# Kernel tuning notes

Hardware: AMD Instinct MI355X
Metric: run time of the kernel (lower is better)

Reference implementation:

```python
import jax, jax.numpy as jnp
import numpy as np

N_NODES = 50000
N_EDGES = 640000
D = 128
N_RELS = 16
N_NTYPES = 8


def setup_inputs() -> dict:
    key = jax.random.key(0)
    ks = jax.random.split(key, 9)
    return {
        "feats": jax.random.normal(ks[0], (N_NODES, D), dtype=jnp.float32),
        "W_edge": jax.random.normal(ks[1], (N_RELS, D, D), dtype=jnp.float32) / np.sqrt(D),
        "b_edge": jax.random.normal(ks[2], (N_RELS, D), dtype=jnp.float32) * 0.02,
        "W_node": jax.random.normal(ks[3], (N_NTYPES, D, D), dtype=jnp.float32) / np.sqrt(D),
        "b_node": jax.random.normal(ks[4], (N_NTYPES, D), dtype=jnp.float32) * 0.02,
        "src": jax.random.randint(ks[5], (N_EDGES,), 0, N_NODES, dtype=jnp.int32),
        "dst": jax.random.randint(ks[6], (N_EDGES,), 0, N_NODES, dtype=jnp.int32),
        "ntypes": jax.random.randint(ks[7], (N_NODES,), 0, N_NTYPES, dtype=jnp.int32),
        "etypes": jax.random.randint(ks[8], (N_EDGES,), 0, N_RELS, dtype=jnp.int32),
    }


def reference(feats, W_edge, b_edge, W_node, b_node, src, dst, ntypes, etypes):
    N, d = feats.shape
    T = W_edge.shape[0]
    # Per-relation linear applied to all nodes once: [T, N, out]; then gather per edge.
    hW = jnp.einsum('nd,tdf->tnf', feats, W_edge) + b_edge[:, None, :]
    msg = hW[etypes, src]  # [E, out]
    # Per-(dst-node, edge-type) in-degree counts (one_hot count normalization).
    seg = dst * T + etypes  # [E]
    counts = jax.ops.segment_sum(jnp.ones(msg.shape[0], dtype=msg.dtype), seg,
                                 num_segments=N * T)  # [N*T]
    msg = msg / counts[seg][:, None]
    # Scatter-sum messages into destination nodes (zero for isolated nodes).
    agg = jax.ops.segment_sum(msg, dst, num_segments=N)  # [N, out]
    # Type-conditional node transform + residual message + activation.
    hN = jnp.einsum('nd,tdf->tnf', feats, W_node) + b_node[:, None, :]  # [Tn, N, out]
    out = hN[ntypes, jnp.arange(N)] + agg
    return jax.nn.relu(out)
```

## Files before the change

kernel.cpp:

```cpp
#include <hip/hip_runtime.h>
#include <hip/hip_bf16.h>
#include <stdint.h>


#define D 128
#define TRELS 16
#define NTYPES 8

typedef __bf16 bf16x8 __attribute__((ext_vector_type(8)));
typedef float f32x4 __attribute__((ext_vector_type(4)));
typedef unsigned int u32x4 __attribute__((ext_vector_type(4)));

__device__ __forceinline__ unsigned short f2bf(float f) {
  union { float f; unsigned u; } v; v.f = f;
  unsigned u = v.u;
  return (unsigned short)((u + 0x7FFFu + ((u >> 16) & 1u)) >> 16);
}
__device__ __forceinline__ float bf2f(unsigned short h) {
  union { unsigned u; float f; } v; v.u = ((unsigned)h) << 16;
  return v.f;
}

__global__ void prep_k(const float* __restrict__ feats,
                       const float* __restrict__ We,
                       const float* __restrict__ Wn,
                       unsigned short* __restrict__ featsbf,
                       unsigned short* __restrict__ WeT,
                       unsigned short* __restrict__ WnT,
                       int nfeat) {
  int idx = blockIdx.x * 256 + threadIdx.x;
  if (idx < nfeat) { featsbf[idx] = f2bf(feats[idx]); return; }
  idx -= nfeat;
  if (idx < TRELS * D * D) {
    int t = idx >> 14, rem = idx & 16383;
    int n = rem >> 7, k = rem & 127;
    WeT[idx] = f2bf(We[t * 16384 + k * 128 + n]);
    return;
  }
  idx -= TRELS * D * D;
  if (idx < NTYPES * D * D) {
    int t = idx >> 14, rem = idx & 16383;
    int n = rem >> 7, k = rem & 127;
    WnT[idx] = f2bf(Wn[t * 16384 + k * 128 + n]);
  }
}

__global__ void hist_k(const int* __restrict__ src, const int* __restrict__ dst,
                       const int* __restrict__ etypes,
                       const int* __restrict__ ntypes, int E, int N,
                       int* __restrict__ cnt, int* __restrict__ nhist,
                       int* __restrict__ srcuse) {
  __shared__ int sh_n[NTYPES];
  int tid = threadIdx.x;
  if (tid < NTYPES) sh_n[tid] = 0;
  __syncthreads();
  int g = blockIdx.x * 256 + tid;
  if (g < E) {
    int et = etypes[g];
    atomicAdd(&cnt[dst[g] * TRELS + et], 1);
    atomicOr(&srcuse[src[g]], 1 << et);
  }
  if (g < N) atomicAdd(&sh_n[ntypes[g]], 1);
  __syncthreads();
  if (tid < NTYPES && sh_n[tid]) atomicAdd(&nhist[tid], sh_n[tid]);
}

__global__ void scan1_k(const int* __restrict__ cnt, int* __restrict__ doff,
                        int* __restrict__ bsum, int N) {
  __shared__ int sd[256];
  int b = blockIdx.x, tid = threadIdx.x;
  int base = b * 1024 + tid * 4;
  int v[4]; int tot = 0;
  for (int j = 0; j < 4; ++j) {
    int i = base + j;
    int dg = 0;
    if (i < N) {
      const int* row = cnt + i * TRELS;
#pragma unroll
      for (int et = 0; et < TRELS; ++et) dg += row[et];
    }
    v[j] = tot; tot += dg;
  }
  sd[tid] = tot;
  __syncthreads();
  for (int off = 1; off < 256; off <<= 1) {
    int t = (tid >= off) ? sd[tid - off] : 0;
    __syncthreads();
    sd[tid] += t;
    __syncthreads();
  }
  int excl = sd[tid] - tot;
  for (int j = 0; j < 4; ++j) {
    int i = base + j;
    if (i < N) doff[i] = excl + v[j];
  }
  if (tid == 255) bsum[b] = sd[255];
}

__global__ void scan2_k(int* __restrict__ misc, int* __restrict__ bsum, int nb) {
  if (threadIdx.x != 0) return;
  int run = 0;
  for (int b = 0; b < nb; ++b) { int t = bsum[b]; bsum[b] = run; run += t; }
  int* noff = misc; int* ntb = misc + 9; int* ncur = misc + 18; int* nhist = misc + 26;
  int s = 0, ts = 0;
  for (int t = 0; t < NTYPES; ++t) {
    noff[t] = s; ncur[t] = s; ntb[t] = ts;
    s += nhist[t]; ts += (nhist[t] + 127) >> 7;
  }
  noff[NTYPES] = s; ntb[NTYPES] = ts;
}

__global__ void scan3_k(int* __restrict__ doff, int* __restrict__ dcur,
                        const int* __restrict__ bsum, int N, int E) {
  int b = blockIdx.x, tid = threadIdx.x;
  int add = bsum[b];
  int base = b * 1024 + tid * 4;
  for (int j = 0; j < 4; ++j) {
    int i = base + j;
    if (i < N) { int o = doff[i] + add; doff[i] = o; dcur[i] = o; }
  }
  if (b == 0 && tid == 0) doff[N] = E;
}

__global__ void scatter_k(const int* __restrict__ src, const int* __restrict__ dst,
                          const int* __restrict__ etypes, const int* __restrict__ ntypes,
                          int E, int N, int* __restrict__ misc,
                          int* __restrict__ dcur,
                          int* __restrict__ edst, int* __restrict__ nsorted) {
  __shared__ int lc_n[NTYPES], lb_n[NTYPES];
  int tid = threadIdx.x;
  if (tid < NTYPES) lc_n[tid] = 0;
  __syncthreads();
  int g = blockIdx.x * 256 + tid;
  if (g < E) {
    int d = dst[g];
    int pos = atomicAdd(&dcur[d], 1);
    edst[pos] = src[g] * TRELS + etypes[g];
  }
  int tn = -1, idn = 0;
  if (g < N) { tn = ntypes[g]; idn = atomicAdd(&lc_n[tn], 1); }
  __syncthreads();
  if (tid < NTYPES && lc_n[tid]) lb_n[tid] = atomicAdd(&misc[18 + tid], lc_n[tid]);
  __syncthreads();
  if (g < N) nsorted[lb_n[tn] + idn] = g;
}

__global__ __launch_bounds__(256) void hw_gemm_k(
    const unsigned short* __restrict__ featsbf,
    const unsigned short* __restrict__ WeT,
    const int* __restrict__ srcuse,
    unsigned short* __restrict__ hW, int N, int mtiles) {
  __shared__ unsigned char Asm[128 * 264];
  __shared__ unsigned char sm_use[128];
  int tid = threadIdx.x;

  int G = mtiles * 16;
  int q = G >> 3, rmod = G & 7;
  int xcd = blockIdx.x & 7, bidx = blockIdx.x >> 3;
  int wrk = (xcd < rmod) ? (xcd * (q + 1) + bidx)
                         : (rmod * (q + 1) + (xcd - rmod) * q + bidx);
  int tile = wrk >> 4;
  int et = wrk & 15;

  int lane = tid & 63, w = tid >> 6;
  int m = lane & 15, qd = lane >> 4;
  int rw = (w & 1) * 64, cw = (w >> 1) * 64;

  const unsigned short* WB = WeT + (size_t)et * (D * D);
  bf16x8 bfr[4][4];
#pragma unroll
  for (int ks = 0; ks < 4; ++ks)
#pragma unroll
    for (int j = 0; j < 4; ++j)
      bfr[ks][j] = *reinterpret_cast<const bf16x8*>(WB + (cw + j * 16 + m) * D + ks * 32 + qd * 8);

  if (tid < 128) {
    int rowu = tile * 128 + tid;
    sm_use[tid] = (rowu < N) ? (unsigned char)((srcuse[rowu] >> et) & 1) : 0;
  }

  int r = tid >> 1, h = tid & 1;
  int row = tile * 128 + r;
  if (row < N) {
    const u32x4* gp = reinterpret_cast<const u32x4*>(featsbf + (size_t)row * D);
#pragma unroll
    for (int cc = 0; cc < 8; ++cc) {
      int c = h * 8 + cc;
      *reinterpret_cast<u32x4*>(&Asm[r * 256 + ((c ^ (r & 7)) << 4)]) = gp[c];
    }
  }
  __syncthreads();

  f32x4 acc[4][4];
#pragma unroll
  for (int i = 0; i < 4; ++i)
#pragma unroll
    for (int j = 0; j < 4; ++j) acc[i][j] = (f32x4){0.f, 0.f, 0.f, 0.f};

#pragma unroll
  for (int ks = 0; ks < 4; ++ks) {
    bf16x8 a[4];
#pragma unroll
    for (int i = 0; i < 4; ++i) {
      int rr = rw + i * 16 + m;
      int c = ks * 4 + qd;
      a[i] = *reinterpret_cast<const bf16x8*>(&Asm[rr * 256 + ((c ^ (rr & 7)) << 4)]);
    }
#pragma unroll
    for (int i = 0; i < 4; ++i)
#pragma unroll
      for (int j = 0; j < 4; ++j)
        acc[i][j] = __builtin_amdgcn_mfma_f32_16x16x32_bf16(a[i], bfr[ks][j], acc[i][j], 0, 0, 0);
  }

  __syncthreads();
  unsigned short* Cs = reinterpret_cast<unsigned short*>(Asm);
#pragma unroll
  for (int i = 0; i < 4; ++i)
#pragma unroll
    for (int j = 0; j < 4; ++j)
#pragma unroll
      for (int reg = 0; reg < 4; ++reg) {
        int rr = rw + i * 16 + qd * 4 + reg;
        Cs[rr * 132 + cw + j * 16 + m] = f2bf(acc[i][j][reg]);
      }
  __syncthreads();
  char* gout = (char*)(hW + ((size_t)et * N + (size_t)tile * 128) * D);
#pragma unroll
  for (int cp = 0; cp < 8; ++cp) {
    int o = cp * 4096 + tid * 16;
    int rloc = o >> 8;
    if (tile * 128 + rloc < N && sm_use[rloc]) {
      u32x4 v = *reinterpret_cast<const u32x4*>(&Asm[rloc * 264 + (o & 255)]);
      *reinterpret_cast<u32x4*>(gout + o) = v;
    }
  }
}

__global__ __launch_bounds__(256) void agg_k(
    const unsigned short* __restrict__ hW,
    const float* __restrict__ b_edge,
    const int* __restrict__ cnt,
    const int* __restrict__ doff, const int* __restrict__ edst,
    float* __restrict__ agg, int N) {
  int tid = threadIdx.x;
  int lane = tid & 63, w = tid >> 6;
  int d = blockIdx.x * 4 + w;
  if (d >= N) return;

  int cv = 0;
  if (lane < TRELS) cv = cnt[d * TRELS + lane];
  float invl = (cv > 0) ? 1.0f / (float)cv : 0.0f;

  int start = doff[d], end = doff[d + 1];
  float ax = 0.f, ay = 0.f;
  for (int base = start; base < end; base += 64) {
    int key = 0;
    if (base + lane < end) key = edst[base + lane];
    int nchunk = end - base; if (nchunk > 64) nchunk = 64;
    int j = 0;
    for (; j + 4 <= nchunk; j += 4) {
      int k0 = __shfl(key, j, 64), k1 = __shfl(key, j + 1, 64);
      int k2 = __shfl(key, j + 2, 64), k3 = __shfl(key, j + 3, 64);
      float i0 = __shfl(invl, k0 & 15, 64), i1 = __shfl(invl, k1 & 15, 64);
      float i2 = __shfl(invl, k2 & 15, 64), i3 = __shfl(invl, k3 & 15, 64);
      ushort2 h0 = *reinterpret_cast<const ushort2*>(hW + ((size_t)(k0 & 15) * N + (k0 >> 4)) * D + lane * 2);
      ushort2 h1 = *reinterpret_cast<const ushort2*>(hW + ((size_t)(k1 & 15) * N + (k1 >> 4)) * D + lane * 2);
      ushort2 h2 = *reinterpret_cast<const ushort2*>(hW + ((size_t)(k2 & 15) * N + (k2 >> 4)) * D + lane * 2);
      ushort2 h3 = *reinterpret_cast<const ushort2*>(hW + ((size_t)(k3 & 15) * N + (k3 >> 4)) * D + lane * 2);
      ax += i0 * bf2f(h0.x); ay += i0 * bf2f(h0.y);
      ax += i1 * bf2f(h1.x); ay += i1 * bf2f(h1.y);
      ax += i2 * bf2f(h2.x); ay += i2 * bf2f(h2.y);
      ax += i3 * bf2f(h3.x); ay += i3 * bf2f(h3.y);
    }
    for (; j < nchunk; ++j) {
      int k = __shfl(key, j, 64);
      float inv = __shfl(invl, k & 15, 64);
      ushort2 hv = *reinterpret_cast<const ushort2*>(hW + ((size_t)(k & 15) * N + (k >> 4)) * D + lane * 2);
      ax += inv * bf2f(hv.x); ay += inv * bf2f(hv.y);
    }
  }
#pragma unroll
  for (int et = 0; et < TRELS; ++et) {
    int c = __shfl(cv, et, 64);
    if (c > 0) {
      const float* bp = b_edge + et * D + lane * 2;
      ax += bp[0]; ay += bp[1];
    }
  }
  float2* op = reinterpret_cast<float2*>(agg + (size_t)d * D + lane * 2);
  *op = make_float2(ax, ay);
}

__global__ __launch_bounds__(256) void node_gemm_k(
    const unsigned short* __restrict__ featsbf,
    const unsigned short* __restrict__ WnT,
    const float* __restrict__ b_node,
    const int* __restrict__ nsorted, const int* __restrict__ misc,
    const float* __restrict__ agg,
    float* __restrict__ out) {
  __shared__ unsigned char Asm[128 * 264];
  __shared__ int sm_node[128];
  __shared__ int s_ntb[9];
  int tid = threadIdx.x;
  if (tid < 9) s_ntb[tid] = misc[9 + tid];
  __syncthreads();
  int bid = blockIdx.x;
  if (bid >= s_ntb[8]) return;
  int t = 0;
  while (bid >= s_ntb[t + 1]) ++t;
  int tile = bid - s_ntb[t];
  int noff_t = misc[t];
  int cntT = misc[t + 1] - noff_t;

  int lane = tid & 63, w = tid >> 6;
  int m = lane & 15, q = lane >> 4;
  int rw = (w & 1) * 64, cw = (w >> 1) * 64;

  const unsigned short* WB = WnT + t * (D * D);
  bf16x8 bfr[4][4];
#pragma unroll
  for (int ks = 0; ks < 4; ++ks)
#pragma unroll
    for (int j = 0; j < 4; ++j)
      bfr[ks][j] = *reinterpret_cast<const bf16x8*>(WB + (cw + j * 16 + m) * D + ks * 32 + q * 8);

  int r = tid >> 1, h = tid & 1;
  int gidx = tile * 128 + r;
  bool rv = gidx < cntT;
  int node = 0;
  if (rv) node = nsorted[noff_t + gidx];
  if (h == 0) sm_node[r] = rv ? node : -1;
  if (rv) {
    const u32x4* gp = reinterpret_cast<const u32x4*>(featsbf + (size_t)node * D);
#pragma unroll
    for (int cc = 0; cc < 8; ++cc) {
      int c = h * 8 + cc;
      *reinterpret_cast<u32x4*>(&Asm[r * 256 + ((c ^ (r & 7)) << 4)]) = gp[c];
    }
  }
  __syncthreads();

  f32x4 acc[4][4];
#pragma unroll
  for (int i = 0; i < 4; ++i)
#pragma unroll
    for (int j = 0; j < 4; ++j) acc[i][j] = (f32x4){0.f, 0.f, 0.f, 0.f};

#pragma unroll
  for (int ks = 0; ks < 4; ++ks) {
    bf16x8 a[4];
#pragma unroll
    for (int i = 0; i < 4; ++i) {
      int rr = rw + i * 16 + m;
      int c = ks * 4 + q;
      a[i] = *reinterpret_cast<const bf16x8*>(&Asm[rr * 256 + ((c ^ (rr & 7)) << 4)]);
    }
#pragma unroll
    for (int i = 0; i < 4; ++i)
#pragma unroll
      for (int j = 0; j < 4; ++j)
        acc[i][j] = __builtin_amdgcn_mfma_f32_16x16x32_bf16(a[i], bfr[ks][j], acc[i][j], 0, 0, 0);
  }

  const float* bnp = b_node + t * D;
  float* Cf = reinterpret_cast<float*>(Asm);
  __syncthreads();
#pragma unroll
  for (int half = 0; half < 2; ++half) {
    if ((w & 1) == half) {
#pragma unroll
      for (int i = 0; i < 4; ++i)
#pragma unroll
        for (int j = 0; j < 4; ++j)
#pragma unroll
          for (int reg = 0; reg < 4; ++reg) {
            int rl = i * 16 + q * 4 + reg;
            Cf[rl * 132 + cw + j * 16 + m] = acc[i][j][reg];
          }
    }
    __syncthreads();
#pragma unroll
    for (int cp = 0; cp < 8; ++cp) {
      int o = cp * 4096 + tid * 16;
      int rl = o >> 9;
      int nd = sm_node[half * 64 + rl];
      if (nd >= 0) {
        int col = (o & 511) >> 2;
        f32x4 c = *reinterpret_cast<const f32x4*>((char*)Cf + rl * 528 + (o & 511));
        f32x4 a = *reinterpret_cast<const f32x4*>(agg + (size_t)nd * D + col);
        f32x4 b4 = *reinterpret_cast<const f32x4*>(bnp + col);
        f32x4 res;
#pragma unroll
        for (int z = 0; z < 4; ++z) res[z] = fmaxf(c[z] + a[z] + b4[z], 0.f);
        *reinterpret_cast<f32x4*>(out + (size_t)nd * D + col) = res;
      }
    }
    __syncthreads();
  }
}

static inline size_t align256(size_t x) { return (x + 255) & ~(size_t)255; }

extern "C" void kernel_launch(void* const* d_in, const int* in_sizes, int n_in,
                              void* d_out, int out_size, void* d_ws, size_t ws_size,
                              hipStream_t stream) {
  const float* feats  = (const float*)d_in[0];
  const float* W_edge = (const float*)d_in[1];
  const float* b_edge = (const float*)d_in[2];
  const float* W_node = (const float*)d_in[3];
  const float* b_node = (const float*)d_in[4];
  const int* src    = (const int*)d_in[5];
  const int* dst    = (const int*)d_in[6];
  const int* ntypes = (const int*)d_in[7];
  const int* etypes = (const int*)d_in[8];
  int N = in_sizes[0] / D;
  int E = in_sizes[5];

  char* ws = (char*)d_ws;
  size_t o_cnt  = 0;
  size_t o_misc = align256(o_cnt + (size_t)N * TRELS * 4);
  size_t o_su   = align256(o_misc + 512);
  size_t zend   = align256(o_su + (size_t)N * 4);
  size_t o_doff = zend;
  size_t o_dcur = align256(o_doff + (size_t)(N + 1) * 4);
  size_t o_edst = align256(o_dcur + (size_t)N * 4);
  size_t o_ns   = align256(o_edst + (size_t)E * 4);
  size_t o_fb   = align256(o_ns + (size_t)N * 4);
  size_t o_we   = align256(o_fb + (size_t)N * D * 2);
  size_t o_wn   = align256(o_we + (size_t)TRELS * D * D * 2);
  size_t o_agg  = align256(o_wn + (size_t)NTYPES * D * D * 2);
  size_t o_hw   = align256(o_agg + (size_t)N * D * 4);

  int* cnt = (int*)(ws + o_cnt);
  int* misc = (int*)(ws + o_misc);
  int* srcuse = (int*)(ws + o_su);
  int* doff = (int*)(ws + o_doff);
  int* dcur = (int*)(ws + o_dcur);
  int* edst = (int*)(ws + o_edst);
  int* nsorted = (int*)(ws + o_ns);
  unsigned short* featsbf = (unsigned short*)(ws + o_fb);
  unsigned short* WeT = (unsigned short*)(ws + o_we);
  unsigned short* WnT = (unsigned short*)(ws + o_wn);
  float* agg = (float*)(ws + o_agg);
  unsigned short* hW = (unsigned short*)(ws + o_hw);
  int* bsum = misc + 64;

  (void)hipMemsetAsync(ws, 0, zend, stream);

  int nfeat = N * D;
  int ptot = nfeat + TRELS * D * D + NTYPES * D * D;
  prep_k<<<(ptot + 255) / 256, 256, 0, stream>>>(feats, W_edge, W_node, featsbf, WeT, WnT, nfeat);

  int hgrid = ((E > N ? E : N) + 255) / 256;
  hist_k<<<hgrid, 256, 0, stream>>>(src, dst, etypes, ntypes, E, N, cnt, misc + 26, srcuse);

  int nb = (N + 1023) / 1024;
  scan1_k<<<nb, 256, 0, stream>>>(cnt, doff, bsum, N);
  scan2_k<<<1, 64, 0, stream>>>(misc, bsum, nb);
  scan3_k<<<nb, 256, 0, stream>>>(doff, dcur, bsum, N, E);

  scatter_k<<<hgrid, 256, 0, stream>>>(src, dst, etypes, ntypes, E, N, misc, dcur, edst, nsorted);

  int mtiles = (N + 127) / 128;
  hw_gemm_k<<<mtiles * 16, 256, 0, stream>>>(featsbf, WeT, srcuse, hW, N, mtiles);

  agg_k<<<(N + 3) / 4, 256, 0, stream>>>(hW, b_edge, cnt, doff, edst, agg, N);

  int ngrid = mtiles + NTYPES;
  node_gemm_k<<<ngrid, 256, 0, stream>>>(featsbf, WnT, b_node, nsorted, misc, agg, (float*)d_out);
}
```

Before: 349.5 us.

## Fuse edge aggregation into node GEMM with 32-row tiles

Merges the separate aggregation kernel into the node-type GEMM kernel so each block aggregates messages for its 32 type-sorted nodes, keeps the result in shared memory, and adds it in the epilogue. This removes the fp32 agg buffer round trip through global memory and one kernel launch. Tiles shrink from 128 to 32 rows, with the tile-count calculation in the scan kernel adjusted to match. Each wave now handles 8 destination nodes serially and reloads the weight fragments per block. Type-sorted node order also makes the doff/cnt accesses scattered rather than sequential.

```diff
diff --git a/kernel.cpp b/kernel.cpp
--- a/kernel.cpp
+++ b/kernel.cpp
@@ -105,7 +105,7 @@
   int s = 0, ts = 0;
   for (int t = 0; t < NTYPES; ++t) {
     noff[t] = s; ncur[t] = s; ntb[t] = ts;
-    s += nhist[t]; ts += (nhist[t] + 127) >> 7;
+    s += nhist[t]; ts += (nhist[t] + 31) >> 5;
   }
   noff[NTYPES] = s; ntb[NTYPES] = ts;
 }
@@ -237,70 +237,19 @@
   }
 }
 
-__global__ __launch_bounds__(256) void agg_k(
-    const unsigned short* __restrict__ hW,
-    const float* __restrict__ b_edge,
-    const int* __restrict__ cnt,
-    const int* __restrict__ doff, const int* __restrict__ edst,
-    float* __restrict__ agg, int N) {
-  int tid = threadIdx.x;
-  int lane = tid & 63, w = tid >> 6;
-  int d = blockIdx.x * 4 + w;
-  if (d >= N) return;
-
-  int cv = 0;
-  if (lane < TRELS) cv = cnt[d * TRELS + lane];
-  float invl = (cv > 0) ? 1.0f / (float)cv : 0.0f;
-
-  int start = doff[d], end = doff[d + 1];
-  float ax = 0.f, ay = 0.f;
-  for (int base = start; base < end; base += 64) {
-    int key = 0;
-    if (base + lane < end) key = edst[base + lane];
-    int nchunk = end - base; if (nchunk > 64) nchunk = 64;
-    int j = 0;
-    for (; j + 4 <= nchunk; j += 4) {
-      int k0 = __shfl(key, j, 64), k1 = __shfl(key, j + 1, 64);
-      int k2 = __shfl(key, j + 2, 64), k3 = __shfl(key, j + 3, 64);
-      float i0 = __shfl(invl, k0 & 15, 64), i1 = __shfl(invl, k1 & 15, 64);
-      float i2 = __shfl(invl, k2 & 15, 64), i3 = __shfl(invl, k3 & 15, 64);
-      ushort2 h0 = *reinterpret_cast<const ushort2*>(hW + ((size_t)(k0 & 15) * N + (k0 >> 4)) * D + lane * 2);
-      ushort2 h1 = *reinterpret_cast<const ushort2*>(hW + ((size_t)(k1 & 15) * N + (k1 >> 4)) * D + lane * 2);
-      ushort2 h2 = *reinterpret_cast<const ushort2*>(hW + ((size_t)(k2 & 15) * N + (k2 >> 4)) * D + lane * 2);
-      ushort2 h3 = *reinterpret_cast<const ushort2*>(hW + ((size_t)(k3 & 15) * N + (k3 >> 4)) * D + lane * 2);
-      ax += i0 * bf2f(h0.x); ay += i0 * bf2f(h0.y);
-      ax += i1 * bf2f(h1.x); ay += i1 * bf2f(h1.y);
-      ax += i2 * bf2f(h2.x); ay += i2 * bf2f(h2.y);
-      ax += i3 * bf2f(h3.x); ay += i3 * bf2f(h3.y);
-    }
-    for (; j < nchunk; ++j) {
-      int k = __shfl(key, j, 64);
-      float inv = __shfl(invl, k & 15, 64);
-      ushort2 hv = *reinterpret_cast<const ushort2*>(hW + ((size_t)(k & 15) * N + (k >> 4)) * D + lane * 2);
-      ax += inv * bf2f(hv.x); ay += inv * bf2f(hv.y);
-    }
-  }
-#pragma unroll
-  for (int et = 0; et < TRELS; ++et) {
-    int c = __shfl(cv, et, 64);
-    if (c > 0) {
-      const float* bp = b_edge + et * D + lane * 2;
-      ax += bp[0]; ay += bp[1];
-    }
-  }
-  float2* op = reinterpret_cast<float2*>(agg + (size_t)d * D + lane * 2);
-  *op = make_float2(ax, ay);
-}
-
-__global__ __launch_bounds__(256) void node_gemm_k(
+__global__ __launch_bounds__(256) void na_k(
     const unsigned short* __restrict__ featsbf,
     const unsigned short* __restrict__ WnT,
     const float* __restrict__ b_node,
+    const float* __restrict__ b_edge,
+    const unsigned short* __restrict__ hW,
+    const int* __restrict__ cnt,
+    const int* __restrict__ doff, const int* __restrict__ edst,
     const int* __restrict__ nsorted, const int* __restrict__ misc,
-    const float* __restrict__ agg,
-    float* __restrict__ out) {
-  __shared__ unsigned char Asm[128 * 264];
-  __shared__ int sm_node[128];
+    float* __restrict__ out, int N) {
+  __shared__ unsigned char Asm[32 * 264];
+  __shared__ float aggbuf[32][128];
+  __shared__ int sm_node[32];
   __shared__ int s_ntb[9];
   int tid = threadIdx.x;
   if (tid < 9) s_ntb[tid] = misc[9 + tid];
@@ -315,80 +264,118 @@
 
   int lane = tid & 63, w = tid >> 6;
   int m = lane & 15, q = lane >> 4;
-  int rw = (w & 1) * 64, cw = (w >> 1) * 64;
-
-  const unsigned short* WB = WnT + t * (D * D);
-  bf16x8 bfr[4][4];
-#pragma unroll
-  for (int ks = 0; ks < 4; ++ks)
+  int wr = w >> 1, wc = w & 1;
+
+  if (tid < 32) {
+    int gidx = tile * 32 + tid;
+    sm_node[tid] = (gidx < cntT) ? nsorted[noff_t + gidx] : -1;
+  }
+  __syncthreads();
+
+  {
+    int r = tid >> 3, h = tid & 7;
+    int node = sm_node[r];
+    if (node >= 0) {
+      const u32x4* gp = reinterpret_cast<const u32x4*>(featsbf + (size_t)node * D);
+#pragma unroll
+      for (int cc = 0; cc < 2; ++cc) {
+        int c = h * 2 + cc;
+        *reinterpret_cast<u32x4*>(&Asm[r * 256 + ((c ^ (r & 7)) << 4)]) = gp[c];
+      }
+    }
+  }
+  __syncthreads();
+
+  const unsigned short* WB = WnT + (size_t)t * (D * D);
+  f32x4 acc[4];
+#pragma unroll
+  for (int j = 0; j < 4; ++j) acc[j] = (f32x4){0.f, 0.f, 0.f, 0.f};
+#pragma unroll
+  for (int ks = 0; ks < 4; ++ks) {
+    bf16x8 bfr[4];
 #pragma unroll
     for (int j = 0; j < 4; ++j)
-      bfr[ks][j] = *reinterpret_cast<const bf16x8*>(WB + (cw + j * 16 + m) * D + ks * 32 + q * 8);
-
-  int r = tid >> 1, h = tid & 1;
-  int gidx = tile * 128 + r;
-  bool rv = gidx < cntT;
-  int node = 0;
-  if (rv) node = nsorted[noff_t + gidx];
-  if (h == 0) sm_node[r] = rv ? node : -1;
-  if (rv) {
-    const u32x4* gp = reinterpret_cast<const u32x4*>(featsbf + (size_t)node * D);
-#pragma unroll
-    for (int cc = 0; cc < 8; ++cc) {
-      int c = h * 8 + cc;
-      *reinterpret_cast<u32x4*>(&Asm[r * 256 + ((c ^ (r & 7)) << 4)]) = gp[c];
-    }
-  }
-  __syncthreads();
-
-  f32x4 acc[4][4];
-#pragma unroll
-  for (int i = 0; i < 4; ++i)
-#pragma unroll
-    for (int j = 0; j < 4; ++j) acc[i][j] = (f32x4){0.f, 0.f, 0.f, 0.f};
-
-#pragma unroll
-  for (int ks = 0; ks < 4; ++ks) {
-    bf16x8 a[4];
-#pragma unroll
-    for (int i = 0; i < 4; ++i) {
-      int rr = rw + i * 16 + m;
-      int c = ks * 4 + q;
-      a[i] = *reinterpret_cast<const bf16x8*>(&Asm[rr * 256 + ((c ^ (rr & 7)) << 4)]);
-    }
-#pragma unroll
-    for (int i = 0; i < 4; ++i)
-#pragma unroll
-      for (int j = 0; j < 4; ++j)
-        acc[i][j] = __builtin_amdgcn_mfma_f32_16x16x32_bf16(a[i], bfr[ks][j], acc[i][j], 0, 0, 0);
-  }
+      bfr[j] = *reinterpret_cast<const bf16x8*>(WB + (wc * 64 + j * 16 + m) * D + ks * 32 + q * 8);
+    int rr = wr * 16 + m;
+    int c = ks * 4 + q;
+    bf16x8 a = *reinterpret_cast<const bf16x8*>(&Asm[rr * 256 + ((c ^ (rr & 7)) << 4)]);
+#pragma unroll
+    for (int j = 0; j < 4; ++j)
+      acc[j] = __builtin_amdgcn_mfma_f32_16x16x32_bf16(a, bfr[j], acc[j], 0, 0, 0);
+  }
+
+  for (int widx = 0; widx < 8; ++widx) {
+    int dloc = w * 8 + widx;
+    int d = sm_node[dloc];
+    if (d < 0) continue;
+    int cv = 0;
+    if (lane < TRELS) cv = cnt[d * TRELS + lane];
+    float invl = (cv > 0) ? 1.0f / (float)cv : 0.0f;
+    int start = doff[d], end = doff[d + 1];
+    float ax = 0.f, ay = 0.f;
+    for (int base = start; base < end; base += 64) {
+      int key = 0;
+      if (base + lane < end) key = edst[base + lane];
+      int nchunk = end - base; if (nchunk > 64) nchunk = 64;
+      int j = 0;
+      for (; j + 4 <= nchunk; j += 4) {
+        int k0 = __shfl(key, j, 64), k1 = __shfl(key, j + 1, 64);
+        int k2 = __shfl(key, j + 2, 64), k3 = __shfl(key, j + 3, 64);
+        float i0 = __shfl(invl, k0 & 15, 64), i1 = __shfl(invl, k1 & 15, 64);
+        float i2 = __shfl(invl, k2 & 15, 64), i3 = __shfl(invl, k3 & 15, 64);
+        ushort2 h0 = *reinterpret_cast<const ushort2*>(hW + ((size_t)(k0 & 15) * N + (k0 >> 4)) * D + lane * 2);
+        ushort2 h1 = *reinterpret_cast<const ushort2*>(hW + ((size_t)(k1 & 15) * N + (k1 >> 4)) * D + lane * 2);
+        ushort2 h2 = *reinterpret_cast<const ushort2*>(hW + ((size_t)(k2 & 15) * N + (k2 >> 4)) * D + lane * 2);
+        ushort2 h3 = *reinterpret_cast<const ushort2*>(hW + ((size_t)(k3 & 15) * N + (k3 >> 4)) * D + lane * 2);
+        ax += i0 * bf2f(h0.x); ay += i0 * bf2f(h0.y);
+        ax += i1 * bf2f(h1.x); ay += i1 * bf2f(h1.y);
+        ax += i2 * bf2f(h2.x); ay += i2 * bf2f(h2.y);
+        ax += i3 * bf2f(h3.x); ay += i3 * bf2f(h3.y);
+      }
+      for (; j < nchunk; ++j) {
+        int k = __shfl(key, j, 64);
+        float inv = __shfl(invl, k & 15, 64);
+        ushort2 hv = *reinterpret_cast<const ushort2*>(hW + ((size_t)(k & 15) * N + (k >> 4)) * D + lane * 2);
+        ax += inv * bf2f(hv.x); ay += inv * bf2f(hv.y);
+      }
+    }
+#pragma unroll
+    for (int et = 0; et < TRELS; ++et) {
+      int c2 = __shfl(cv, et, 64);
+      if (c2 > 0) {
+        const float* bp = b_edge + et * D + lane * 2;
+        ax += bp[0]; ay += bp[1];
+      }
+    }
+    aggbuf[dloc][lane * 2] = ax;
+    aggbuf[dloc][lane * 2 + 1] = ay;
+  }
+  __syncthreads();
 
   const float* bnp = b_node + t * D;
   float* Cf = reinterpret_cast<float*>(Asm);
-  __syncthreads();
 #pragma unroll
   for (int half = 0; half < 2; ++half) {
-    if ((w & 1) == half) {
-#pragma unroll
-      for (int i = 0; i < 4; ++i)
-#pragma unroll
-        for (int j = 0; j < 4; ++j)
-#pragma unroll
-          for (int reg = 0; reg < 4; ++reg) {
-            int rl = i * 16 + q * 4 + reg;
-            Cf[rl * 132 + cw + j * 16 + m] = acc[i][j][reg];
-          }
+    if (wr == half) {
+#pragma unroll
+      for (int j = 0; j < 4; ++j)
+#pragma unroll
+        for (int reg = 0; reg < 4; ++reg) {
+          int rl = q * 4 + reg;
+          Cf[rl * 132 + wc * 64 + j * 16 + m] = acc[j][reg];
+        }
     }
     __syncthreads();
 #pragma unroll
-    for (int cp = 0; cp < 8; ++cp) {
+    for (int cp = 0; cp < 2; ++cp) {
       int o = cp * 4096 + tid * 16;
       int rl = o >> 9;
-      int nd = sm_node[half * 64 + rl];
+      int dl = half * 16 + rl;
+      int nd = sm_node[dl];
       if (nd >= 0) {
         int col = (o & 511) >> 2;
         f32x4 c = *reinterpret_cast<const f32x4*>((char*)Cf + rl * 528 + (o & 511));
-        f32x4 a = *reinterpret_cast<const f32x4*>(agg + (size_t)nd * D + col);
+        f32x4 a = *reinterpret_cast<const f32x4*>(&aggbuf[dl][col]);
         f32x4 b4 = *reinterpret_cast<const f32x4*>(bnp + col);
         f32x4 res;
 #pragma unroll
@@ -429,8 +416,7 @@
   size_t o_fb   = align256(o_ns + (size_t)N * 4);
   size_t o_we   = align256(o_fb + (size_t)N * D * 2);
   size_t o_wn   = align256(o_we + (size_t)TRELS * D * D * 2);
-  size_t o_agg  = align256(o_wn + (size_t)NTYPES * D * D * 2);
-  size_t o_hw   = align256(o_agg + (size_t)N * D * 4);
+  size_t o_hw   = align256(o_wn + (size_t)NTYPES * D * D * 2);
 
   int* cnt = (int*)(ws + o_cnt);
   int* misc = (int*)(ws + o_misc);
@@ -442,7 +428,6 @@
   unsigned short* featsbf = (unsigned short*)(ws + o_fb);
   unsigned short* WeT = (unsigned short*)(ws + o_we);
   unsigned short* WnT = (unsigned short*)(ws + o_wn);
-  float* agg = (float*)(ws + o_agg);
   unsigned short* hW = (unsigned short*)(ws + o_hw);
   int* bsum = misc + 64;
 
@@ -465,8 +450,7 @@
   int mtiles = (N + 127) / 128;
   hw_gemm_k<<<mtiles * 16, 256, 0, stream>>>(featsbf, WeT, srcuse, hW, N, mtiles);
 
-  agg_k<<<(N + 3) / 4, 256, 0, stream>>>(hW, b_edge, cnt, doff, edst, agg, N);
-
-  int ngrid = mtiles + NTYPES;
-  node_gemm_k<<<ngrid, 256, 0, stream>>>(featsbf, WnT, b_node, nsorted, misc, agg, (float*)d_out);
-}
+  int ngrid = (N + 31) / 32 + NTYPES;
+  na_k<<<ngrid, 256, 0, stream>>>(featsbf, WnT, b_node, b_edge, hW, cnt, doff, edst,
+                                  nsorted, misc, (float*)d_out, N);
+}
```

Result: slower. 395.0 us (+13.0%).
